# Optimization experiments

Measured on AMD Instinct MI355X. Metric: run time of the kernel, lower is better.

The kernel has to match this reference:

```python
import jax, jax.numpy as jnp
import numpy as np

B, S, D, H = 4, 2048, 768, 12
HD = D // H  # 64


def setup_inputs() -> dict:
    key = jax.random.key(0)
    ks = jax.random.split(key, 6)
    sc = 0.02
    return {
        "x": jax.random.normal(ks[0], (B, S, D), dtype=jnp.float32),
        "wq": jax.random.normal(ks[1], (D, D), dtype=jnp.float32) * sc,
        "wk": jax.random.normal(ks[2], (D, D), dtype=jnp.float32) * sc,
        "wv": jax.random.normal(ks[3], (D, D), dtype=jnp.float32) * sc,
        "wo": jax.random.normal(ks[4], (D, D), dtype=jnp.float32) * sc,
        "bo": jnp.zeros((D,), dtype=jnp.float32),
    }


def reference(x, wq, wk, wv, wo, bo):
    b, s, d = x.shape
    # nn.Linear applies x @ W^T; project then split heads -> [b, h, s, hd]
    def heads(w):
        return (x @ w.T).reshape(b, s, H, HD).transpose(0, 2, 1, 3)
    q, k, v = heads(wq), heads(wk), heads(wv)
    scores = jnp.einsum("bhqd,bhkd->bhqk", q, k)
    causal = jnp.triu(jnp.ones((s, s), dtype=bool), 1)
    # original masks with -inf BEFORE scaling; -inf/sqrt(d) == -inf, same softmax
    scores = jnp.where(causal, -jnp.inf, scores) / jnp.sqrt(jnp.float32(HD))
    attn = jax.nn.softmax(scores, axis=-1)  # dropout=0.0 (eval/deterministic)
    ctx = jnp.einsum("bhqk,bhkd->bhqd", attn, v)
    ctx = ctx.transpose(0, 2, 1, 3).reshape(b, s, d)
    return ctx @ wo.T + bo
```

## Files before the change

kernel.cpp:

```cpp
#include <hip/hip_runtime.h>

#define B_ 4
#define S_ 2048
#define D_ 768
#define H_ 12
#define HD_ 64
#define T_ (B_ * S_)

typedef __bf16 bf16x8 __attribute__((ext_vector_type(8)));
typedef __bf16 bf16x4 __attribute__((ext_vector_type(4)));
typedef float  f32x4  __attribute__((ext_vector_type(4)));

__device__ __forceinline__ f32x4 mfma16(bf16x8 a, bf16x8 b, f32x4 c) {
  return __builtin_amdgcn_mfma_f32_16x16x32_bf16(a, b, c, 0, 0, 0);
}

__device__ __forceinline__ float fexp2(float x) {
  float r;
  asm("v_exp_f32 %0, %1" : "=v"(r) : "v"(x));
  return r;
}

__device__ __forceinline__ void gload16(const __bf16* g, __bf16* lds) {
  __builtin_amdgcn_global_load_lds(
      (__attribute__((address_space(1))) void*)g,
      (__attribute__((address_space(3))) void*)lds, 16, 0, 0);
}

__global__ void cvt_all(const float* __restrict__ x,
                        const float* __restrict__ wq,
                        const float* __restrict__ wk,
                        const float* __restrict__ wv,
                        const float* __restrict__ wo,
                        __bf16* __restrict__ out) {
  constexpr int XN4 = T_ * D_ / 4;
  constexpr int WN4 = D_ * D_ / 4;
  const int i = blockIdx.x * blockDim.x + threadIdx.x;
  if (i >= XN4 + 4 * WN4) return;
  const float* src;
  int k;
  float scale = 1.0f;
  if (i < XN4) {
    src = x;
    k = i;
  } else {
    const int j = i - XN4;
    const int wsel = j / WN4;
    k = j - wsel * WN4;
    src = (wsel == 0) ? wq : (wsel == 1) ? wk : (wsel == 2) ? wv : wo;
    if (wsel == 1) scale = 0.18033688f;
  }
  const float4 v = reinterpret_cast<const float4*>(src)[k];
  bf16x4 o;
  o[0] = (__bf16)(v.x * scale);
  o[1] = (__bf16)(v.y * scale);
  o[2] = (__bf16)(v.z * scale);
  o[3] = (__bf16)(v.w * scale);
  reinterpret_cast<bf16x4*>(out)[i] = o;
}

template <int MODE>
__global__ __launch_bounds__(256)
__attribute__((amdgpu_waves_per_eu(2)))
void gemm_bt(const __bf16* __restrict__ A,
             const __bf16* __restrict__ W0, const __bf16* __restrict__ W1,
             const __bf16* __restrict__ W2,
             __bf16* __restrict__ Oq, __bf16* __restrict__ Ok,
             __bf16* __restrict__ Ov,
             float* __restrict__ fout, const float* __restrict__ bias) {
  constexpr int K = D_;
  constexpr int NT = K / 64;
  __shared__ __align__(16) char smem[65536];
  __bf16* sA0 = reinterpret_cast<__bf16*>(smem);
  __bf16* sB0 = reinterpret_cast<__bf16*>(smem + 32768);

  const int tid = threadIdx.x;
  const int l = tid & 63;
  const int w = tid >> 6;

  const int flat = blockIdx.y * 64 + blockIdx.x;
  const int xcd = flat & 7;
  const int q = flat >> 3;
  const int mtile = xcd * 8 + (q & 7);
  const int pan = q >> 3;
  const int m0 = mtile * 128;

  int mat, n0;
  const __bf16* Wm;
  if (MODE == 0) {
    mat = pan / 6;
    n0 = (pan % 6) * 128;
    Wm = (mat == 0) ? W0 : (mat == 1) ? W1 : W2;
  } else {
    mat = 0;
    n0 = pan * 128;
    Wm = W0;
  }

  const int srow = l >> 3;
  const int scol = ((l & 7) ^ srow) * 8;
  const __bf16* gA[4];
  const __bf16* gB[4];
#pragma unroll
  for (int i = 0; i < 4; ++i) {
    const int c = w * 4 + i;
    gA[i] = A + (size_t)(m0 + c * 8 + srow) * K + scol;
    gB[i] = Wm + (size_t)(n0 + c * 8 + srow) * K + scol;
  }

  f32x4 acc[4][4] = {};
  const int wr = w >> 1, wc = w & 1;
  const int fr = l & 15, fq = l >> 4;
  const int swz = (fr & 7) << 4;

#pragma unroll
  for (int i = 0; i < 4; ++i) {
    const int c = w * 4 + i;
    gload16(gA[i], &sA0[c * 512]);
    gload16(gB[i], &sB0[c * 512]);
  }
#pragma unroll
  for (int i = 0; i < 4; ++i) {
    const int c = w * 4 + i;
    gload16(gA[i] + 64, &sA0[8192 + c * 512]);
    gload16(gB[i] + 64, &sB0[8192 + c * 512]);
  }

  int cur = 0;
  for (int kt = 0; kt < NT; ++kt) {
    if (kt + 1 < NT)
      asm volatile("s_waitcnt vmcnt(8)" ::: "memory");
    else
      asm volatile("s_waitcnt vmcnt(0)" ::: "memory");
    __builtin_amdgcn_s_barrier();

    const char* ab = reinterpret_cast<const char*>(&sA0[cur * 8192]);
    const char* bb = reinterpret_cast<const char*>(&sB0[cur * 8192]);
#pragma unroll
    for (int ks = 0; ks < 2; ++ks) {
      bf16x8 af[4], bfr[4];
#pragma unroll
      for (int mi = 0; mi < 4; ++mi)
        af[mi] = *reinterpret_cast<const bf16x8*>(
            ab + (wr * 64 + mi * 16 + fr) * 128 +
            ((ks * 64 + fq * 16) ^ swz));
#pragma unroll
      for (int ni = 0; ni < 4; ++ni)
        bfr[ni] = *reinterpret_cast<const bf16x8*>(
            bb + (wc * 64 + ni * 16 + fr) * 128 +
            ((ks * 64 + fq * 16) ^ swz));
#pragma unroll
      for (int mi = 0; mi < 4; ++mi)
#pragma unroll
        for (int ni = 0; ni < 4; ++ni)
          acc[mi][ni] = mfma16(af[mi], bfr[ni], acc[mi][ni]);
    }
    __builtin_amdgcn_s_barrier();

    if (kt + 2 < NT) {
      const int ko = (kt + 2) * 64;
#pragma unroll
      for (int i = 0; i < 4; ++i) {
        const int c = w * 4 + i;
        gload16(gA[i] + ko, &sA0[cur * 8192 + c * 512]);
        gload16(gB[i] + ko, &sB0[cur * 8192 + c * 512]);
      }
    }
    cur ^= 1;
  }

  if (MODE == 0 && mat == 2) {
#pragma unroll
    for (int mi = 0; mi < 4; ++mi) {
      const int mbase = m0 + wr * 64 + mi * 16 + fq * 4;
      const int b = mbase >> 11, s = mbase & (S_ - 1);
#pragma unroll
      for (int ni = 0; ni < 4; ++ni) {
        const int o = n0 + wc * 64 + ni * 16 + fr;
        const int h = o >> 6, hd = o & 63;
        bf16x4 vv;
#pragma unroll
        for (int r = 0; r < 4; ++r) vv[r] = (__bf16)acc[mi][ni][r];
        *reinterpret_cast<bf16x4*>(
            &Ov[((size_t)((b * H_ + h) * HD_ + hd)) * S_ + s]) = vv;
      }
    }
  } else {
    float* fW = reinterpret_cast<float*>(smem) + w * 4096;
#pragma unroll
    for (int mi = 0; mi < 4; ++mi)
#pragma unroll
      for (int ni = 0; ni < 4; ++ni)
#pragma unroll
        for (int r = 0; r < 4; ++r)
          fW[(mi * 16 + fq * 4 + r) * 64 + ni * 16 + fr] = acc[mi][ni][r];
    if (MODE == 1) {
      const int ocol = n0 + wc * 64 + fr * 4;
      const float4 bs = *reinterpret_cast<const float4*>(&bias[ocol]);
#pragma unroll
      for (int it = 0; it < 16; ++it) {
        const int lrow = it * 4 + fq;
        f32x4 v = *reinterpret_cast<const f32x4*>(&fW[lrow * 64 + fr * 4]);
        v[0] += bs.x;
        v[1] += bs.y;
        v[2] += bs.z;
        v[3] += bs.w;
        *reinterpret_cast<f32x4*>(
            &fout[(size_t)(m0 + wr * 64 + lrow) * D_ + ocol]) = v;
      }
    } else {
      const int o = n0 + wc * 64;
      const int h = o >> 6;
      __bf16* dst = (mat == 0) ? Oq : Ok;
#pragma unroll
      for (int it = 0; it < 16; ++it) {
        const int lrow = it * 4 + fq;
        const int m = m0 + wr * 64 + lrow;
        const int b = m >> 11, s = m & (S_ - 1);
        const f32x4 v =
            *reinterpret_cast<const f32x4*>(&fW[lrow * 64 + fr * 4]);
        bf16x4 ov;
#pragma unroll
        for (int r = 0; r < 4; ++r) ov[r] = (__bf16)v[r];
        *reinterpret_cast<bf16x4*>(
            &dst[((size_t)((b * H_ + h) * S_ + s)) * HD_ + fr * 4]) = ov;
      }
    }
  }
}

__global__ __launch_bounds__(256)
__attribute__((amdgpu_waves_per_eu(4, 4)))
void attn_kernel(const __bf16* __restrict__ Q, const __bf16* __restrict__ Kt,
                 const __bf16* __restrict__ Vt, __bf16* __restrict__ C) {
  __shared__ __align__(16) __bf16 sK[2][64 * 64];
  __shared__ __align__(16) __bf16 sV[2][64 * 64];
  __shared__ __align__(16) __bf16 sP[4][16 * 64];

  const int tid = threadIdx.x;
  const int l = tid & 63;
  const int w = tid >> 6;
  const int fr = l & 15, fq = l >> 4;
  const int bx = blockIdx.x;
  const int xcd = bx & 7;
  const int j = bx >> 3;
  const int bh = xcd + 8 * (j % 6);
  const int qtile = 31 - j / 6;
  const int qb = qtile * 64;
  const int qbw = qb + w * 16;

  const __bf16* qh = Q + (size_t)bh * S_ * HD_;
  const __bf16* kh = Kt + (size_t)bh * S_ * HD_;
  const __bf16* vh = Vt + (size_t)bh * HD_ * S_;
  char* sPb = reinterpret_cast<char*>(&sP[w][0]);

  const int srow = l >> 3;
  const int scol = ((l & 7) * 8) ^ (srow << 3);
  const int swz = (fr & 7) << 4;

  bf16x8 qf[2];
#pragma unroll
  for (int ks = 0; ks < 2; ++ks)
    qf[ks] = *reinterpret_cast<const bf16x8*>(
        &qh[(size_t)(qbw + fr) * HD_ + ks * 32 + fq * 8]);

  f32x4 acc[4] = {};
  float mrow = -1e30f, lrow = 0.f;

  const int nt = qtile + 1;
  int cur = 0;
  const int q0 = 2 * w, q1 = 2 * w + 1;

  gload16(kh + (size_t)(q0 * 8 + srow) * HD_ + scol, &sK[0][q0 * 512]);
  gload16(kh + (size_t)(q1 * 8 + srow) * HD_ + scol, &sK[0][q1 * 512]);
  gload16(vh + (size_t)(q0 * 8 + srow) * S_ + scol, &sV[0][q0 * 512]);
  gload16(vh + (size_t)(q1 * 8 + srow) * S_ + scol, &sV[0][q1 * 512]);
  if (nt > 1) {
    gload16(kh + (size_t)(64 + q0 * 8 + srow) * HD_ + scol, &sK[1][q0 * 512]);
    gload16(kh + (size_t)(64 + q1 * 8 + srow) * HD_ + scol, &sK[1][q1 * 512]);
    gload16(vh + (size_t)(q0 * 8 + srow) * S_ + 64 + scol, &sV[1][q0 * 512]);
    gload16(vh + (size_t)(q1 * 8 + srow) * S_ + 64 + scol, &sV[1][q1 * 512]);
  }

  for (int t = 0; t < nt; ++t) {
    if (t + 1 < nt)
      asm volatile("s_waitcnt vmcnt(4)" ::: "memory");
    else
      asm volatile("s_waitcnt vmcnt(0)" ::: "memory");
    __builtin_amdgcn_s_barrier();

    const int kv0 = t * 64;
    if (kv0 <= qbw + 15) {
      const char* kb = reinterpret_cast<const char*>(&sK[cur][0]);
      const char* vb = reinterpret_cast<const char*>(&sV[cur][0]);

      f32x4 s[4];
      __builtin_amdgcn_s_setprio(1);
#pragma unroll
      for (int c = 0; c < 4; ++c) {
        const int row = c * 16 + fr;
        bf16x8 kf0 = *reinterpret_cast<const bf16x8*>(
            kb + row * 128 + ((fq * 16) ^ swz));
        bf16x8 kf1 = *reinterpret_cast<const bf16x8*>(
            kb + row * 128 + ((fq * 16 + 64) ^ swz));
        f32x4 z = {};
        z = mfma16(kf0, qf[0], z);
        z = mfma16(kf1, qf[1], z);
        s[c] = z;
      }
      __builtin_amdgcn_s_setprio(0);

      if (kv0 + 63 > qbw) {
        const int qi = qbw + fr;
#pragma unroll
        for (int c = 0; c < 4; ++c)
#pragma unroll
          for (int r = 0; r < 4; ++r) {
            const int kvi = kv0 + c * 16 + fq * 4 + r;
            if (kvi > qi) s[c][r] = -1e30f;
          }
      }

      float tm = -1e30f;
#pragma unroll
      for (int c = 0; c < 4; ++c)
#pragma unroll
        for (int r = 0; r < 4; ++r) tm = fmaxf(tm, s[c][r]);
      tm = fmaxf(tm, __shfl_xor(tm, 16));
      tm = fmaxf(tm, __shfl_xor(tm, 32));
      const float mn = fmaxf(mrow, tm);
      const float fac = fexp2(mrow - mn);
      mrow = mn;
      float sum = 0.f;
#pragma unroll
      for (int c = 0; c < 4; ++c) {
        bf16x4 pc;
#pragma unroll
        for (int r = 0; r < 4; ++r) {
          const float p = fexp2(s[c][r] - mn);
          sum += p;
          pc[r] = (__bf16)p;
        }
        const int bo = (c * 32 + fq * 8) ^ swz;
        *reinterpret_cast<bf16x4*>(sPb + fr * 128 + bo) = pc;
      }
      sum += __shfl_xor(sum, 16);
      sum += __shfl_xor(sum, 32);
      lrow = lrow * fac + sum;
#pragma unroll
      for (int dt = 0; dt < 4; ++dt)
#pragma unroll
        for (int r = 0; r < 4; ++r) acc[dt][r] *= fac;

      bf16x8 pa[2];
#pragma unroll
      for (int ks = 0; ks < 2; ++ks) {
        const int bo = (ks * 64 + fq * 16) ^ swz;
        pa[ks] = *reinterpret_cast<const bf16x8*>(sPb + fr * 128 + bo);
      }

      __builtin_amdgcn_s_setprio(1);
#pragma unroll
      for (int dt = 0; dt < 4; ++dt) {
        const int row = dt * 16 + fr;
        bf16x8 vf0 = *reinterpret_cast<const bf16x8*>(
            vb + row * 128 + ((fq * 16) ^ swz));
        bf16x8 vf1 = *reinterpret_cast<const bf16x8*>(
            vb + row * 128 + ((fq * 16 + 64) ^ swz));
        acc[dt] = mfma16(vf0, pa[0], acc[dt]);
        acc[dt] = mfma16(vf1, pa[1], acc[dt]);
      }
      __builtin_amdgcn_s_setprio(0);
    }

    __builtin_amdgcn_s_barrier();

    if (t + 2 < nt) {
      const int kvn = (t + 2) * 64;
      gload16(kh + (size_t)(kvn + q0 * 8 + srow) * HD_ + scol,
              &sK[cur][q0 * 512]);
      gload16(kh + (size_t)(kvn + q1 * 8 + srow) * HD_ + scol,
              &sK[cur][q1 * 512]);
      gload16(vh + (size_t)(q0 * 8 + srow) * S_ + kvn + scol,
              &sV[cur][q0 * 512]);
      gload16(vh + (size_t)(q1 * 8 + srow) * S_ + kvn + scol,
              &sV[cur][q1 * 512]);
    }
    cur ^= 1;
  }

  const int b = bh / H_, h = bh % H_;
  const float inv_l = 1.0f / lrow;
  const int qrow = qbw + fr;
#pragma unroll
  for (int dt = 0; dt < 4; ++dt) {
    bf16x4 ov;
#pragma unroll
    for (int r = 0; r < 4; ++r) ov[r] = (__bf16)(acc[dt][r] * inv_l);
    *reinterpret_cast<bf16x4*>(
        &C[((size_t)(b * S_ + qrow)) * D_ + h * HD_ + dt * 16 + fq * 4]) = ov;
  }
}

static constexpr size_t XB_OFF = 0;
static constexpr size_t WQ_OFF = XB_OFF + (size_t)T_ * D_;
static constexpr size_t WK_OFF = WQ_OFF + (size_t)D_ * D_;
static constexpr size_t WV_OFF = WK_OFF + (size_t)D_ * D_;
static constexpr size_t WO_OFF = WV_OFF + (size_t)D_ * D_;
static constexpr size_t Q_OFF = WO_OFF + (size_t)D_ * D_;
static constexpr size_t K_OFF = Q_OFF + (size_t)T_ * D_;
static constexpr size_t V_OFF = K_OFF + (size_t)T_ * D_;
static constexpr size_t C_OFF = V_OFF + (size_t)T_ * D_;

extern "C" void kernel_launch(void* const* d_in, const int* in_sizes, int n_in,
                              void* d_out, int out_size, void* d_ws,
                              size_t ws_size, hipStream_t stream) {
  const float* x = (const float*)d_in[0];
  const float* wq = (const float*)d_in[1];
  const float* wk = (const float*)d_in[2];
  const float* wv = (const float*)d_in[3];
  const float* wo = (const float*)d_in[4];
  const float* bo = (const float*)d_in[5];
  float* out = (float*)d_out;
  __bf16* ws = (__bf16*)d_ws;

  __bf16* xb = ws + XB_OFF;
  __bf16* wqb = ws + WQ_OFF;
  __bf16* wkb = ws + WK_OFF;
  __bf16* wvb = ws + WV_OFF;
  __bf16* wob = ws + WO_OFF;
  __bf16* qbuf = ws + Q_OFF;
  __bf16* kbuf = ws + K_OFF;
  __bf16* vbuf = ws + V_OFF;
  __bf16* cbuf = ws + C_OFF;

  {
    constexpr int n4 = T_ * D_ / 4 + 4 * (D_ * D_ / 4);
    cvt_all<<<(n4 + 255) / 256, 256, 0, stream>>>(x, wq, wk, wv, wo, ws);
  }

  gemm_bt<0><<<dim3(64, 18), 256, 0, stream>>>(
      xb, wqb, wkb, wvb, qbuf, kbuf, vbuf, nullptr, nullptr);

  attn_kernel<<<dim3(1536), 256, 0, stream>>>(qbuf, kbuf, vbuf, cbuf);

  gemm_bt<1><<<dim3(64, 6), 256, 0, stream>>>(
      cbuf, wob, nullptr, nullptr, nullptr, nullptr, nullptr, out, bo);
}
```

Baseline: 117.7 us.

## Load GEMM weight fragments directly to registers and defer softmax rescaling

The projection GEMM no longer stages the weight tile in LDS. Each wave loads its B fragments from global memory straight into double-buffered registers, which halves the shared memory footprint, and the epilogue is split into two halves to fit the smaller LDS. In attention, the running-max rescale of the accumulators and row sum is skipped when every lane's new tile max exceeds the old max by at most 8 in the log2 domain. This trades LDS use and rescale ALU work for more VGPR pressure, uncoalesced-style global loads for weights, and a bounded growth of the exponentials.

New measurement: 161.1 us. 36.8% more time.

```diff
diff --git a/kernel.cpp b/kernel.cpp
--- a/kernel.cpp
+++ b/kernel.cpp
@@ -70,9 +70,8 @@
              float* __restrict__ fout, const float* __restrict__ bias) {
   constexpr int K = D_;
   constexpr int NT = K / 64;
-  __shared__ __align__(16) char smem[65536];
+  __shared__ __align__(16) char smem[32768];
   __bf16* sA0 = reinterpret_cast<__bf16*>(smem);
-  __bf16* sB0 = reinterpret_cast<__bf16*>(smem + 32768);
 
   const int tid = threadIdx.x;
   const int l = tid & 63;
@@ -100,12 +99,10 @@
   const int srow = l >> 3;
   const int scol = ((l & 7) ^ srow) * 8;
   const __bf16* gA[4];
-  const __bf16* gB[4];
 #pragma unroll
   for (int i = 0; i < 4; ++i) {
     const int c = w * 4 + i;
     gA[i] = A + (size_t)(m0 + c * 8 + srow) * K + scol;
-    gB[i] = Wm + (size_t)(n0 + c * 8 + srow) * K + scol;
   }
 
   f32x4 acc[4][4] = {};
@@ -113,61 +110,58 @@
   const int fr = l & 15, fq = l >> 4;
   const int swz = (fr & 7) << 4;
 
-#pragma unroll
-  for (int i = 0; i < 4; ++i) {
-    const int c = w * 4 + i;
-    gload16(gA[i], &sA0[c * 512]);
-    gload16(gB[i], &sB0[c * 512]);
-  }
-#pragma unroll
-  for (int i = 0; i < 4; ++i) {
-    const int c = w * 4 + i;
-    gload16(gA[i] + 64, &sA0[8192 + c * 512]);
-    gload16(gB[i] + 64, &sB0[8192 + c * 512]);
-  }
-
-  int cur = 0;
-  for (int kt = 0; kt < NT; ++kt) {
-    if (kt + 1 < NT)
-      asm volatile("s_waitcnt vmcnt(8)" ::: "memory");
-    else
-      asm volatile("s_waitcnt vmcnt(0)" ::: "memory");
-    __builtin_amdgcn_s_barrier();
-
-    const char* ab = reinterpret_cast<const char*>(&sA0[cur * 8192]);
-    const char* bb = reinterpret_cast<const char*>(&sB0[cur * 8192]);
-#pragma unroll
-    for (int ks = 0; ks < 2; ++ks) {
-      bf16x8 af[4], bfr[4];
-#pragma unroll
-      for (int mi = 0; mi < 4; ++mi)
-        af[mi] = *reinterpret_cast<const bf16x8*>(
-            ab + (wr * 64 + mi * 16 + fr) * 128 +
-            ((ks * 64 + fq * 16) ^ swz));
-#pragma unroll
-      for (int ni = 0; ni < 4; ++ni)
-        bfr[ni] = *reinterpret_cast<const bf16x8*>(
-            bb + (wc * 64 + ni * 16 + fr) * 128 +
-            ((ks * 64 + fq * 16) ^ swz));
-#pragma unroll
-      for (int mi = 0; mi < 4; ++mi)
-#pragma unroll
-        for (int ni = 0; ni < 4; ++ni)
-          acc[mi][ni] = mfma16(af[mi], bfr[ni], acc[mi][ni]);
-    }
-    __builtin_amdgcn_s_barrier();
-
-    if (kt + 2 < NT) {
-      const int ko = (kt + 2) * 64;
-#pragma unroll
-      for (int i = 0; i < 4; ++i) {
-        const int c = w * 4 + i;
-        gload16(gA[i] + ko, &sA0[cur * 8192 + c * 512]);
-        gload16(gB[i] + ko, &sB0[cur * 8192 + c * 512]);
-      }
-    }
-    cur ^= 1;
-  }
+  const __bf16* bp = Wm + (size_t)(n0 + wc * 64 + fr) * K + fq * 8;
+
+#pragma unroll
+  for (int i = 0; i < 4; ++i) gload16(gA[i], &sA0[(w * 4 + i) * 512]);
+#pragma unroll
+  for (int i = 0; i < 4; ++i)
+    gload16(gA[i] + 64, &sA0[8192 + (w * 4 + i) * 512]);
+  bf16x8 bfA[4][2], bfB[4][2];
+#pragma unroll
+  for (int ni = 0; ni < 4; ++ni)
+#pragma unroll
+    for (int ks = 0; ks < 2; ++ks)
+      bfA[ni][ks] = *reinterpret_cast<const bf16x8*>(
+          bp + (size_t)(ni * 16) * K + ks * 32);
+
+#define GEMM_BODY(KT, SB, BFC, BFN)                                          \
+  do {                                                                       \
+    if ((KT) + 1 < NT)                                                       \
+      asm volatile("s_waitcnt vmcnt(12)" ::: "memory");                      \
+    else                                                                     \
+      asm volatile("s_waitcnt vmcnt(8)" ::: "memory");                       \
+    __builtin_amdgcn_s_barrier();                                            \
+    if ((KT) + 1 < NT) {                                                     \
+      _Pragma("unroll") for (int ni = 0; ni < 4; ++ni)                       \
+          _Pragma("unroll") for (int ks = 0; ks < 2; ++ks)                   \
+              BFN[ni][ks] = *reinterpret_cast<const bf16x8*>(                \
+                  bp + (size_t)(ni * 16) * K + ((KT) + 1) * 64 + ks * 32);   \
+    }                                                                        \
+    const char* ab = reinterpret_cast<const char*>(&sA0[(SB)*8192]);         \
+    _Pragma("unroll") for (int ks = 0; ks < 2; ++ks) {                       \
+      bf16x8 af[4];                                                          \
+      _Pragma("unroll") for (int mi = 0; mi < 4; ++mi) af[mi] =              \
+          *reinterpret_cast<const bf16x8*>(ab +                              \
+                                           (wr * 64 + mi * 16 + fr) * 128 +  \
+                                           ((ks * 64 + fq * 16) ^ swz));     \
+      _Pragma("unroll") for (int mi = 0; mi < 4; ++mi)                       \
+          _Pragma("unroll") for (int ni = 0; ni < 4; ++ni) acc[mi][ni] =     \
+              mfma16(af[mi], BFC[ni][ks], acc[mi][ni]);                      \
+    }                                                                        \
+    __builtin_amdgcn_s_barrier();                                            \
+    if ((KT) + 2 < NT) {                                                     \
+      const int ko = ((KT) + 2) * 64;                                        \
+      _Pragma("unroll") for (int i = 0; i < 4; ++i)                          \
+          gload16(gA[i] + ko, &sA0[(SB)*8192 + (w * 4 + i) * 512]);          \
+    }                                                                        \
+  } while (0)
+
+  for (int kt = 0; kt < NT; kt += 2) {
+    GEMM_BODY(kt, 0, bfA, bfB);
+    GEMM_BODY(kt + 1, 1, bfB, bfA);
+  }
+#undef GEMM_BODY
 
   if (MODE == 0 && mat == 2) {
 #pragma unroll
@@ -186,44 +180,49 @@
       }
     }
   } else {
-    float* fW = reinterpret_cast<float*>(smem) + w * 4096;
-#pragma unroll
-    for (int mi = 0; mi < 4; ++mi)
-#pragma unroll
-      for (int ni = 0; ni < 4; ++ni)
-#pragma unroll
-        for (int r = 0; r < 4; ++r)
-          fW[(mi * 16 + fq * 4 + r) * 64 + ni * 16 + fr] = acc[mi][ni][r];
-    if (MODE == 1) {
-      const int ocol = n0 + wc * 64 + fr * 4;
-      const float4 bs = *reinterpret_cast<const float4*>(&bias[ocol]);
-#pragma unroll
-      for (int it = 0; it < 16; ++it) {
-        const int lrow = it * 4 + fq;
-        f32x4 v = *reinterpret_cast<const f32x4*>(&fW[lrow * 64 + fr * 4]);
-        v[0] += bs.x;
-        v[1] += bs.y;
-        v[2] += bs.z;
-        v[3] += bs.w;
-        *reinterpret_cast<f32x4*>(
-            &fout[(size_t)(m0 + wr * 64 + lrow) * D_ + ocol]) = v;
-      }
-    } else {
-      const int o = n0 + wc * 64;
-      const int h = o >> 6;
-      __bf16* dst = (mat == 0) ? Oq : Ok;
-#pragma unroll
-      for (int it = 0; it < 16; ++it) {
-        const int lrow = it * 4 + fq;
-        const int m = m0 + wr * 64 + lrow;
-        const int b = m >> 11, s = m & (S_ - 1);
-        const f32x4 v =
-            *reinterpret_cast<const f32x4*>(&fW[lrow * 64 + fr * 4]);
-        bf16x4 ov;
-#pragma unroll
-        for (int r = 0; r < 4; ++r) ov[r] = (__bf16)v[r];
-        *reinterpret_cast<bf16x4*>(
-            &dst[((size_t)((b * H_ + h) * S_ + s)) * HD_ + fr * 4]) = ov;
+    float* fW = reinterpret_cast<float*>(smem) + w * 2048;
+#pragma unroll
+    for (int half = 0; half < 2; ++half) {
+#pragma unroll
+      for (int mi2 = 0; mi2 < 2; ++mi2)
+#pragma unroll
+        for (int ni = 0; ni < 4; ++ni)
+#pragma unroll
+          for (int r = 0; r < 4; ++r)
+            fW[(mi2 * 16 + fq * 4 + r) * 64 + ni * 16 + fr] =
+                acc[half * 2 + mi2][ni][r];
+      if (MODE == 1) {
+        const int ocol = n0 + wc * 64 + fr * 4;
+        const float4 bs = *reinterpret_cast<const float4*>(&bias[ocol]);
+#pragma unroll
+        for (int it = 0; it < 8; ++it) {
+          const int lrow = it * 4 + fq;
+          f32x4 v = *reinterpret_cast<const f32x4*>(&fW[lrow * 64 + fr * 4]);
+          v[0] += bs.x;
+          v[1] += bs.y;
+          v[2] += bs.z;
+          v[3] += bs.w;
+          *reinterpret_cast<f32x4*>(
+              &fout[(size_t)(m0 + wr * 64 + half * 32 + lrow) * D_ + ocol]) =
+              v;
+        }
+      } else {
+        const int o = n0 + wc * 64;
+        const int h = o >> 6;
+        __bf16* dst = (mat == 0) ? Oq : Ok;
+#pragma unroll
+        for (int it = 0; it < 8; ++it) {
+          const int lrow = it * 4 + fq;
+          const int m = m0 + wr * 64 + half * 32 + lrow;
+          const int b = m >> 11, s = m & (S_ - 1);
+          const f32x4 v =
+              *reinterpret_cast<const f32x4*>(&fW[lrow * 64 + fr * 4]);
+          bf16x4 ov;
+#pragma unroll
+          for (int r = 0; r < 4; ++r) ov[r] = (__bf16)v[r];
+          *reinterpret_cast<bf16x4*>(
+              &dst[((size_t)((b * H_ + h) * S_ + s)) * HD_ + fr * 4]) = ov;
+        }
       }
     }
   }
@@ -328,9 +327,17 @@
         for (int r = 0; r < 4; ++r) tm = fmaxf(tm, s[c][r]);
       tm = fmaxf(tm, __shfl_xor(tm, 16));
       tm = fmaxf(tm, __shfl_xor(tm, 32));
-      const float mn = fmaxf(mrow, tm);
-      const float fac = fexp2(mrow - mn);
-      mrow = mn;
+      const bool defer = __all(tm - mrow <= 8.0f);
+      const float mn = defer ? mrow : fmaxf(mrow, tm);
+      if (!defer) {
+        const float fac = fexp2(mrow - mn);
+        mrow = mn;
+        lrow *= fac;
+#pragma unroll
+        for (int dt = 0; dt < 4; ++dt)
+#pragma unroll
+          for (int r = 0; r < 4; ++r) acc[dt][r] *= fac;
+      }
       float sum = 0.f;
 #pragma unroll
       for (int c = 0; c < 4; ++c) {
@@ -346,11 +353,7 @@
       }
       sum += __shfl_xor(sum, 16);
       sum += __shfl_xor(sum, 32);
-      lrow = lrow * fac + sum;
-#pragma unroll
-      for (int dt = 0; dt < 4; ++dt)
-#pragma unroll
-        for (int r = 0; r < 4; ++r) acc[dt][r] *= fac;
+      lrow += sum;
 
       bf16x8 pa[2];
 #pragma unroll
```
